# Performance work log

Measured on AMD Instinct MI355X. Metric: run time of the kernel, lower is better.

The kernel has to match this reference:

```python
import jax, jax.numpy as jnp
import numpy as np

EPS_BN = 1e-5
EPS_LN = 1e-5

def _bn(x, g, b, m, v):
    # inference-mode BatchNorm2d over channel dim 1
    scale = g / jnp.sqrt(v + EPS_BN)
    return x * scale[None, :, None, None] + (b - m * scale)[None, :, None, None]

def _conv1x1(x, w, b=None):
    y = jnp.einsum('bchw,oc->bohw', x, w)
    if b is not None:
        y = y + b[None, :, None, None]
    return y

def _gelu(x):
    return jax.nn.gelu(x, approximate=False)

def setup_inputs() -> dict:
    key = jax.random.key(0)
    ks = jax.random.split(key, 40)
    B, C, H, W = 32, 160, 56, 56
    C5, C3 = C // 5, C * 3
    s = 0.05
    d = {}
    d['x'] = jax.random.normal(ks[0], (B, C, H, W), jnp.float32)
    d['bn1_g'] = jax.random.uniform(ks[1], (C,), jnp.float32, 0.5, 1.5)
    d['bn1_b'] = jax.random.normal(ks[2], (C,)) * s
    d['bn1_m'] = jax.random.normal(ks[3], (C,)) * s
    d['bn1_v'] = jnp.ones((C,), jnp.float32)
    names = ['t', 'b', 'r', 'l', 'c']
    for i, n in enumerate(names):
        d['w' + n] = jax.random.normal(ks[4 + i], (C5, C)) * s
        d['b' + n] = jax.random.normal(ks[9 + i], (C5,)) * s
    d['wf1'] = jax.random.normal(ks[14], (C, C)) * s
    d['bf1'] = jax.random.normal(ks[15], (C,)) * s
    d['bn2_g'] = jax.random.uniform(ks[16], (C,), jnp.float32, 0.5, 1.5)
    d['bn2_b'] = jax.random.normal(ks[17], (C,)) * s
    d['bn2_m'] = jax.random.normal(ks[18], (C,)) * s
    d['bn2_v'] = jnp.ones((C,), jnp.float32)
    d['wph'] = jax.random.normal(ks[19], (W, W)) * s
    d['bph'] = jax.random.normal(ks[20], (W,)) * s
    d['wpw'] = jax.random.normal(ks[21], (H, H)) * s
    d['bpw'] = jax.random.normal(ks[22], (H,)) * s
    d['wf2'] = jax.random.normal(ks[23], (C, C3)) * s
    d['ln_g'] = jax.random.uniform(ks[24], (C,), jnp.float32, 0.5, 1.5)
    d['ln_b'] = jax.random.normal(ks[25], (C,)) * s
    d['wfc1'] = jax.random.normal(ks[26], (C3, C)) * s
    d['bfc1'] = jax.random.normal(ks[27], (C3,)) * s
    d['wfc2'] = jax.random.normal(ks[28], (C, C3)) * s
    d['bfc2'] = jax.random.normal(ks[29], (C,)) * s
    d['step'] = 1
    return d

def reference(x, bn1_g, bn1_b, bn1_m, bn1_v, wt, bt, wb, bb, wr, br, wl, bl, wc, bc,
              wf1, bf1, bn2_g, bn2_b, bn2_m, bn2_v, wph, bph, wpw, bpw, wf2,
              ln_g, ln_b, wfc1, bfc1, wfc2, bfc2, step):
    B, C, H, W = x.shape
    # ---- localMix: ShiftedPillarsConcatentation_BNAct_NP5 ----
    h = _gelu(_bn(x, bn1_g, bn1_b, bn1_m, bn1_v))
    x_t = _conv1x1(h, wt, bt)
    x_b = _conv1x1(h, wb, bb)
    x_r = _conv1x1(h, wr, br)
    x_l = _conv1x1(h, wl, bl)
    x_c = _conv1x1(h, wc, bc)
    # pad then narrow exactly as torch: t/l shift by 1, b/r shift by step
    x_t = jnp.pad(x_t, ((0, 0), (0, 0), (0, step), (0, 0)))[:, :, 1:1 + H, :]
    x_b = jnp.pad(x_b, ((0, 0), (0, 0), (step, 0), (0, 0)))[:, :, 0:H, :]
    x_l = jnp.pad(x_l, ((0, 0), (0, 0), (0, 0), (0, step)))[:, :, :, 1:1 + W]
    x_r = jnp.pad(x_r, ((0, 0), (0, 0), (0, 0), (step, 0)))[:, :, :, 0:W]
    lm = _conv1x1(jnp.concatenate([x_t, x_b, x_r, x_l, x_c], axis=1), wf1, bf1)
    # ---- globalMix: sparseMLP_BNAct ----
    g = _gelu(_bn(lm, bn2_g, bn2_b, bn2_m, bn2_v))
    # proj_h mixes the W axis (input permuted to (B,W,C,H)), bias per output W
    x_h = jnp.einsum('bchw,vw->bchv', g, wph) + bph[None, None, None, :]
    # proj_w mixes the H axis (input permuted to (B,H,C,W)), bias per output H
    x_w = jnp.einsum('bchw,uh->bcuw', g, wpw) + bpw[None, None, :, None]
    gm = _conv1x1(jnp.concatenate([g, x_h, x_w], axis=1), wf2)  # no bias
    x1 = gm + x  # residual 1
    # ---- channelMix: LN + Mlp over channels ----
    y = jnp.transpose(x1, (0, 2, 3, 1))  # BHWC
    mu = jnp.mean(y, axis=-1, keepdims=True)
    var = jnp.mean(jnp.square(y - mu), axis=-1, keepdims=True)
    y = (y - mu) / jnp.sqrt(var + EPS_LN) * ln_g + ln_b
    y = _gelu(jnp.einsum('bhwc,fc->bhwf', y, wfc1) + bfc1)
    y = jnp.einsum('bhwf,cf->bhwc', y, wfc2) + bfc2
    return jnp.transpose(y, (0, 3, 1, 2)) + x1  # residual 2
```

## Files before the change

kernel.cpp:

```cpp
#include <hip/hip_runtime.h>
#include <hip/hip_bf16.h>
#include <math.h>

typedef __hip_bfloat16 bf16;
typedef __attribute__((ext_vector_type(8))) short s8v;
typedef __attribute__((ext_vector_type(4))) float f4v;

#define Bn  32
#define Cn  160
#define HWn 3136
#define Pn  100352

__device__ __forceinline__ float b2f(bf16 v){ return __bfloat162float(v); }
__device__ __forceinline__ bf16  f2b(float v){ return __float2bfloat16(v); }
__device__ __forceinline__ float bits2f(unsigned short u){
    union { float f; unsigned int i; } x; x.i = ((unsigned int)u) << 16; return x.f;
}
__device__ __forceinline__ float gelu_f(float x){ return 0.5f*x*(1.0f + erff(x*0.7071067811865476f)); }

#define MFMA(a,b,c) __builtin_amdgcn_mfma_f32_16x16x32_bf16((a),(b),(c),0,0,0)

__global__ __launch_bounds__(256) void k0_prep(
    const float* __restrict__ wt, const float* __restrict__ wb_, const float* __restrict__ wr,
    const float* __restrict__ wl, const float* __restrict__ wc,
    const float* __restrict__ bt, const float* __restrict__ bb_, const float* __restrict__ br,
    const float* __restrict__ bl, const float* __restrict__ bc,
    const float* __restrict__ wf1, const float* __restrict__ bf1,
    const float* __restrict__ g2, const float* __restrict__ b2, const float* __restrict__ m2, const float* __restrict__ v2,
    const float* __restrict__ wf2, const float* __restrict__ wfc1, const float* __restrict__ wfc2,
    const float* __restrict__ wph, const float* __restrict__ wpw,
    const float* __restrict__ lng, const float* __restrict__ lnb, const float* __restrict__ bfc1,
    bf16* wcat, bf16* wf1b, bf16* wf2b, bf16* wfc1g, bf16* wfc2b, bf16* wphb, bf16* wpwb,
    float* bcat, float* epsv, float* eptv, float* wgs, float* wcb)
{
    int idx = blockIdx.x*256 + threadIdx.x;
    if (idx < 25600){ int o = idx/160, k = idx - o*160; int gi = o>>5, oo = o&31;
        const float* wp = gi==0?wt: gi==1?wb_: gi==2?wr: gi==3?wl: wc;
        wcat[idx] = f2b(wp[oo*160+k]); return; }
    idx -= 25600;
    if (idx < 25600){ wf1b[idx] = f2b(wf1[idx]); return; }
    idx -= 25600;
    if (idx < 76800){ wf2b[idx] = f2b(wf2[idx]); return; }
    idx -= 76800;
    if (idx < 76800){ int f = idx/160, c = idx - f*160;
        wfc1g[idx] = f2b(wfc1[f*160+c] * lng[c]); return; }
    idx -= 76800;
    if (idx < 76800){ wfc2b[idx] = f2b(wfc2[idx]); return; }
    idx -= 76800;
    if (idx < 4096){ int v = idx>>6, w = idx&63;
        wphb[idx] = (v<56 && w<56) ? f2b(wph[v*56+w]) : f2b(0.f); return; }
    idx -= 4096;
    if (idx < 4096){ int v = idx>>6, w = idx&63;
        wpwb[idx] = (v<56 && w<56) ? f2b(wpw[v*56+w]) : f2b(0.f); return; }
    idx -= 4096;
    if (idx < 160){ int o = idx; int gi = o>>5, oo = o&31;
        const float* bp = gi==0?bt: gi==1?bb_: gi==2?br: gi==3?bl: bc;
        bcat[o] = bp[oo]; return; }
    idx -= 160;
    if (idx < 160){ int o = idx; float s = g2[o]*rsqrtf(v2[o]+1e-5f);
        epsv[o] = s; eptv[o] = (bf1[o]-m2[o])*s + b2[o]; return; }
    idx -= 160;
    if (idx < 480){ int o = idx; float sg = 0.f, sb = 0.f;
        const float* wr_ = wfc1 + (size_t)o*160;
        for (int c = 0; c < 160; ++c){ float w = wr_[c]; sg += w*lng[c]; sb += w*lnb[c]; }
        wgs[o] = sg; wcb[o] = sb + bfc1[o]; return; }
}

__global__ __launch_bounds__(256) void k1_bn_gelu_tr(const float* __restrict__ x,
    const float* __restrict__ g, const float* __restrict__ b,
    const float* __restrict__ m, const float* __restrict__ v,
    bf16* __restrict__ hT)
{
    __shared__ float tile[64*161];
    __shared__ float sc[160], sh[160];
    int blk = blockIdx.x; int bb = blk/49; int hw0 = (blk - bb*49)*64;
    int tid = threadIdx.x;
    if (tid < 160){
        float s = g[tid] * rsqrtf(v[tid] + 1e-5f);
        sc[tid] = s; sh[tid] = b[tid] - m[tid]*s;
    }
    __syncthreads();
    const float* xb = x + (size_t)bb*Cn*HWn + hw0;
    for (int idx = tid; idx < 160*64; idx += 256){
        int c = idx >> 6, p = idx & 63;
        float val = xb[(size_t)c*HWn + p];
        tile[p*161 + c] = gelu_f(val*sc[c] + sh[c]);
    }
    __syncthreads();
    bf16* ho = hT + ((size_t)bb*HWn + hw0)*Cn;
    for (int idx = tid; idx < 64*160; idx += 256){
        int p = idx/160, c = idx - p*160;
        ho[idx] = f2b(tile[p*161 + c]);
    }
}

__global__ __launch_bounds__(256) void k2_conv5(const bf16* __restrict__ hT,
    const bf16* __restrict__ wcat, const float* __restrict__ bcat, bf16* __restrict__ y5T)
{
    __shared__ __align__(16) unsigned short Bs[2][16*168];
    int tid = threadIdx.x, wave = tid>>6, lane = tid&63, m = lane&15, q = lane>>4;
    size_t pos0 = (size_t)blockIdx.x*64;
    const unsigned short* Ap = (const unsigned short*)hT + (pos0 + wave*16 + m)*160 + q*8;
    s8v a[5];
    #pragma unroll
    for (int kb = 0; kb < 5; ++kb) a[kb] = *(const s8v*)(Ap + kb*32);
    { const s8v* sp = (const s8v*)((const unsigned short*)wcat);
      for (int c = tid; c < 320; c += 256){ int row = c/20, col = (c - row*20)*8;
          *(s8v*)&Bs[0][row*168 + col] = sp[c]; } }
    __syncthreads();
    for (int s = 0; s < 10; ++s){
        if (s+1 < 10){
            const s8v* sp = (const s8v*)((const unsigned short*)wcat + (size_t)(s+1)*2560);
            for (int c = tid; c < 320; c += 256){ int row = c/20, col = (c - row*20)*8;
                *(s8v*)&Bs[(s+1)&1][row*168 + col] = sp[c]; }
        }
        f4v acc = {0.f,0.f,0.f,0.f};
        const unsigned short* Bp = &Bs[s&1][m*168 + q*8];
        #pragma unroll
        for (int kb = 0; kb < 5; ++kb) acc = MFMA(a[kb], *(const s8v*)(Bp + kb*32), acc);
        float bias = bcat[s*16 + m];
        bf16* yo = y5T + (pos0 + wave*16 + q*4)*160 + s*16 + m;
        #pragma unroll
        for (int r = 0; r < 4; ++r) yo[r*160] = f2b(acc[r] + bias);
        __syncthreads();
    }
}

__global__ __launch_bounds__(256) void k3_wf1(const bf16* __restrict__ y5T,
    const bf16* __restrict__ wf1b, const float* __restrict__ epsv, const float* __restrict__ eptv,
    bf16* __restrict__ gT)
{
    __shared__ __align__(16) unsigned short Bs[2][16*168];
    int tid = threadIdx.x, wave = tid>>6, lane = tid&63, m = lane&15, q = lane>>4;
    int blk = blockIdx.x; int bb = blk/49; int hw0 = (blk - bb*49)*64;
    size_t pos0 = (size_t)bb*HWn + hw0;
    int phw = hw0 + wave*16 + m; int h = phw/56, w = phw - h*56;
    s8v a[5];
    #pragma unroll
    for (int kb = 0; kb < 5; ++kb){
        int h2 = h, w2 = w; bool ok = true;
        if      (kb == 0){ h2 = h+1; ok = (h2 < 56); }
        else if (kb == 1){ h2 = h-1; ok = (h2 >= 0); }
        else if (kb == 2){ w2 = w-1; ok = (w2 >= 0); }
        else if (kb == 3){ w2 = w+1; ok = (w2 < 56); }
        if (ok){
            const unsigned short* Ap = (const unsigned short*)y5T +
                ((size_t)bb*HWn + h2*56 + w2)*160 + kb*32 + q*8;
            a[kb] = *(const s8v*)Ap;
        } else {
            a[kb] = (s8v){0,0,0,0,0,0,0,0};
        }
    }
    { const s8v* sp = (const s8v*)((const unsigned short*)wf1b);
      for (int c = tid; c < 320; c += 256){ int row = c/20, col = (c - row*20)*8;
          *(s8v*)&Bs[0][row*168 + col] = sp[c]; } }
    __syncthreads();
    for (int s = 0; s < 10; ++s){
        if (s+1 < 10){
            const s8v* sp = (const s8v*)((const unsigned short*)wf1b + (size_t)(s+1)*2560);
            for (int c = tid; c < 320; c += 256){ int row = c/20, col = (c - row*20)*8;
                *(s8v*)&Bs[(s+1)&1][row*168 + col] = sp[c]; }
        }
        f4v acc = {0.f,0.f,0.f,0.f};
        const unsigned short* Bp = &Bs[s&1][m*168 + q*8];
        #pragma unroll
        for (int kb = 0; kb < 5; ++kb) acc = MFMA(a[kb], *(const s8v*)(Bp + kb*32), acc);
        int o = s*16 + m;
        float es = epsv[o], et = eptv[o];
        bf16* go = gT + (pos0 + wave*16 + q*4)*160 + o;
        #pragma unroll
        for (int r = 0; r < 4; ++r) go[r*160] = f2b(gelu_f(acc[r]*es + et));
        __syncthreads();
    }
}

__global__ __launch_bounds__(256) void k4_projh(const bf16* __restrict__ gT,
    const bf16* __restrict__ wphb, const float* __restrict__ bph, bf16* __restrict__ xhT)
{
    __shared__ __align__(16) unsigned short gS[160*72];
    int tid = threadIdx.x, wave = tid>>6, lane = tid&63, m = lane&15, q = lane>>4;
    int blk = blockIdx.x; int b = blk/56, h = blk - b*56;
    const unsigned short* ga = (const unsigned short*)gT + ((size_t)b*HWn + h*56)*160;
    for (int idx = tid; idx < 56*160; idx += 256){
        int w = idx/160, c = idx - w*160;
        gS[c*72 + w] = ga[idx];
    }
    for (int idx = tid; idx < 160*8; idx += 256){
        int c = idx>>3, w = 56 + (idx&7);
        gS[c*72 + w] = 0;
    }
    __syncthreads();
    int v0 = wave*16;
    s8v a[2];
    #pragma unroll
    for (int kb = 0; kb < 2; ++kb)
        a[kb] = *(const s8v*)((const unsigned short*)wphb + (v0+m)*64 + kb*32 + q*8);
    int v = v0 + q*4;
    for (int s = 0; s < 10; ++s){
        f4v acc = {0.f,0.f,0.f,0.f};
        const unsigned short* Bp = &gS[(s*16+m)*72 + q*8];
        #pragma unroll
        for (int kb = 0; kb < 2; ++kb) acc = MFMA(a[kb], *(const s8v*)(Bp + kb*32), acc);
        #pragma unroll
        for (int r = 0; r < 4; ++r){
            int vv = v + r;
            if (vv < 56)
                xhT[((size_t)b*HWn + h*56 + vv)*160 + s*16 + m] = f2b(acc[r] + bph[vv]);
        }
    }
}

__global__ __launch_bounds__(256) void k5_projw(const bf16* __restrict__ gT,
    const bf16* __restrict__ wpwb, const float* __restrict__ bpw, bf16* __restrict__ xwT)
{
    __shared__ __align__(16) unsigned short gS[160*72];
    int tid = threadIdx.x, wave = tid>>6, lane = tid&63, m = lane&15, q = lane>>4;
    int blk = blockIdx.x; int b = blk/56, w = blk - b*56;
    const unsigned short* gbase = (const unsigned short*)gT + ((size_t)b*HWn + w)*160;
    for (int idx = tid; idx < 56*160; idx += 256){
        int hh = idx/160, c = idx - hh*160;
        gS[c*72 + hh] = gbase[(size_t)hh*56*160 + c];
    }
    for (int idx = tid; idx < 160*8; idx += 256){
        int c = idx>>3, hh = 56 + (idx&7);
        gS[c*72 + hh] = 0;
    }
    __syncthreads();
    int v0 = wave*16;
    s8v a[2];
    #pragma unroll
    for (int kb = 0; kb < 2; ++kb)
        a[kb] = *(const s8v*)((const unsigned short*)wpwb + (v0+m)*64 + kb*32 + q*8);
    int v = v0 + q*4;
    for (int s = 0; s < 10; ++s){
        f4v acc = {0.f,0.f,0.f,0.f};
        const unsigned short* Bp = &gS[(s*16+m)*72 + q*8];
        #pragma unroll
        for (int kb = 0; kb < 2; ++kb) acc = MFMA(a[kb], *(const s8v*)(Bp + kb*32), acc);
        #pragma unroll
        for (int r = 0; r < 4; ++r){
            int vv = v + r;
            if (vv < 56)
                xwT[((size_t)b*HWn + vv*56 + w)*160 + s*16 + m] = f2b(acc[r] + bpw[vv]);
        }
    }
}

__global__ __launch_bounds__(256) void k6_wf2(const bf16* __restrict__ gT,
    const bf16* __restrict__ xhT, const bf16* __restrict__ xwT,
    const bf16* __restrict__ wf2b, bf16* __restrict__ gm)
{
    __shared__ __align__(16) unsigned short Bs[2][16*488];
    int tid = threadIdx.x, wave = tid>>6, lane = tid&63, m = lane&15, q = lane>>4;
    size_t pos0 = (size_t)blockIdx.x*64;
    size_t prow = (pos0 + wave*16 + m)*160;
    s8v a[15];
    #pragma unroll
    for (int kb = 0; kb < 15; ++kb){
        const bf16* src = (kb < 5) ? gT : (kb < 10 ? xhT : xwT);
        int kc = (kb - (kb < 5 ? 0 : (kb < 10 ? 5 : 10)))*32 + q*8;
        a[kb] = *(const s8v*)((const unsigned short*)src + prow + kc);
    }
    { const s8v* sp = (const s8v*)((const unsigned short*)wf2b);
      for (int c = tid; c < 960; c += 256){ int row = c/60, col = (c - row*60)*8;
          *(s8v*)&Bs[0][row*488 + col] = sp[c]; } }
    __syncthreads();
    for (int s = 0; s < 10; ++s){
        if (s+1 < 10){
            const s8v* sp = (const s8v*)((const unsigned short*)wf2b + (size_t)(s+1)*7680);
            for (int c = tid; c < 960; c += 256){ int row = c/60, col = (c - row*60)*8;
                *(s8v*)&Bs[(s+1)&1][row*488 + col] = sp[c]; }
        }
        f4v acc = {0.f,0.f,0.f,0.f};
        const unsigned short* Bp = &Bs[s&1][m*488 + q*8];
        #pragma unroll
        for (int kb = 0; kb < 15; ++kb) acc = MFMA(a[kb], *(const s8v*)(Bp + kb*32), acc);
        bf16* go = gm + (pos0 + wave*16 + q*4)*160 + s*16 + m;
        #pragma unroll
        for (int r = 0; r < 4; ++r) go[r*160] = f2b(acc[r]);
        __syncthreads();
    }
}

__global__ __launch_bounds__(256,4) void k7_ln_fc1(const float* __restrict__ x,
    const bf16* __restrict__ gm,
    const bf16* __restrict__ wfc1g, const float* __restrict__ wgs, const float* __restrict__ wcb,
    bf16* __restrict__ u)
{
    __shared__ __align__(16) float XsU[160*64];
    unsigned short* As = (unsigned short*)XsU;
    float* rstd_s = XsU + 5120;
    float* mrs_s  = XsU + 5184;
    int tid = threadIdx.x, wave = tid>>6, lane = tid&63, m = lane&15, q = lane>>4;
    int blk = blockIdx.x; int bb = blk/49; int hw0 = (blk - bb*49)*64;
    size_t pos0 = (size_t)bb*HWn + hw0;
    const float* xb = x + (size_t)bb*Cn*HWn + hw0;
    for (int idx = tid; idx < 160*64; idx += 256){
        int c = idx >> 6, p = idx & 63;
        XsU[idx] = xb[(size_t)c*HWn + p];
    }
    __syncthreads();
    int p = tid >> 2, q4 = tid & 3;
    {
        const s8v* gp = (const s8v*)((const unsigned short*)gm + (pos0 + p)*160 + q4*40);
        float y[40];
        float s = 0.f, ss = 0.f;
        #pragma unroll
        for (int j = 0; j < 5; ++j){
            s8v gv = gp[j];
            #pragma unroll
            for (int t = 0; t < 8; ++t){
                int i = j*8 + t;
                float vv = XsU[(q4*40 + i)*64 + p] + bits2f((unsigned short)gv[t]);
                y[i] = vv; s += vv; ss += vv*vv;
            }
        }
        s  += __shfl_xor(s, 1);  ss += __shfl_xor(ss, 1);
        s  += __shfl_xor(s, 2);  ss += __shfl_xor(ss, 2);
        float mean = s * (1.f/160.f);
        float var  = ss * (1.f/160.f) - mean*mean;
        float rstd = rsqrtf(var + 1e-5f);
        __syncthreads();
        #pragma unroll
        for (int j = 0; j < 5; ++j){
            s8v pk;
            #pragma unroll
            for (int t = 0; t < 8; ++t){
                union { unsigned short us; bf16 b; } cv; cv.b = f2b(y[j*8 + t]);
                pk[t] = (short)cv.us;
            }
            *(s8v*)&As[p*160 + q4*40 + j*8] = pk;
        }
        if (q4 == 0){ rstd_s[p] = rstd; mrs_s[p] = -mean*rstd; }
    }
    __syncthreads();
    s8v a[5];
    const unsigned short* Ap = &As[(wave*16 + m)*160 + q*8];
    #pragma unroll
    for (int kb = 0; kb < 5; ++kb) a[kb] = *(const s8v*)(Ap + kb*32);
    float rst[4], mrs[4];
    #pragma unroll
    for (int r = 0; r < 4; ++r){
        rst[r] = rstd_s[wave*16 + q*4 + r];
        mrs[r] = mrs_s [wave*16 + q*4 + r];
    }
    const unsigned short* Wp = (const unsigned short*)wfc1g + (size_t)m*160 + q*8;
    bf16* uo = u + (pos0 + wave*16 + q*4)*480 + m;
    s8v b0[5], b1[5];
    #pragma unroll
    for (int kb = 0; kb < 5; ++kb) b0[kb] = *(const s8v*)(Wp + kb*32);
    for (int s = 0; s < 30; s += 2){
        {
            const unsigned short* Wn = Wp + (size_t)(s+1)*2560;
            #pragma unroll
            for (int kb = 0; kb < 5; ++kb) b1[kb] = *(const s8v*)(Wn + kb*32);
        }
        f4v acc = {0.f,0.f,0.f,0.f};
        #pragma unroll
        for (int kb = 0; kb < 5; ++kb) acc = MFMA(a[kb], b0[kb], acc);
        {
            int o = s*16 + m; float wg = wgs[o], wc = wcb[o];
            #pragma unroll
            for (int r = 0; r < 4; ++r){
                float v = acc[r]*rst[r] + mrs[r]*wg + wc;
                uo[(size_t)r*480 + s*16] = f2b(gelu_f(v));
            }
        }
        if (s + 2 < 30){
            const unsigned short* Wn = Wp + (size_t)(s+2)*2560;
            #pragma unroll
            for (int kb = 0; kb < 5; ++kb) b0[kb] = *(const s8v*)(Wn + kb*32);
        }
        f4v acc2 = {0.f,0.f,0.f,0.f};
        #pragma unroll
        for (int kb = 0; kb < 5; ++kb) acc2 = MFMA(a[kb], b1[kb], acc2);
        {
            int o = (s+1)*16 + m; float wg = wgs[o], wc = wcb[o];
            #pragma unroll
            for (int r = 0; r < 4; ++r){
                float v = acc2[r]*rst[r] + mrs[r]*wg + wc;
                uo[(size_t)r*480 + (s+1)*16] = f2b(gelu_f(v));
            }
        }
    }
}

__global__ __launch_bounds__(256) void k8_fc2(const bf16* __restrict__ u,
    const bf16* __restrict__ wfc2b, const float* __restrict__ bfc2,
    const float* __restrict__ x, const bf16* __restrict__ gm, float* __restrict__ out)
{
    __shared__ float Ds[64*161];
    __shared__ __align__(16) unsigned short Bs[2][16*488];
    int tid = threadIdx.x, wave = tid>>6, lane = tid&63, m = lane&15, q = lane>>4;
    int blk = blockIdx.x; int bb = blk/49; int hw0 = (blk - bb*49)*64;
    size_t pos0 = (size_t)bb*HWn + hw0;
    const float* xb = x + (size_t)bb*Cn*HWn + hw0;
    for (int idx = tid; idx < 160*64; idx += 256){
        int o = idx >> 6, p = idx & 63;
        Ds[p*161 + o] = xb[(size_t)o*HWn + p];
    }
    { const s8v* sp = (const s8v*)((const unsigned short*)wfc2b);
      for (int c = tid; c < 960; c += 256){ int row = c/60, col = (c - row*60)*8;
          *(s8v*)&Bs[0][row*488 + col] = sp[c]; } }
    __syncthreads();
    {
        const unsigned short* gp = (const unsigned short*)gm + pos0*160;
        for (int idx = tid; idx < 64*160; idx += 256){
            int p = idx/160, c = idx - p*160;
            Ds[p*161 + c] += bits2f(gp[idx]);
        }
    }
    __syncthreads();
    const unsigned short* Ap = (const unsigned short*)u + (pos0 + wave*16 + m)*480 + q*8;
    s8v a[15];
    #pragma unroll
    for (int kb = 0; kb < 15; ++kb) a[kb] = *(const s8v*)(Ap + kb*32);
    for (int s = 0; s < 10; ++s){
        if (s+1 < 10){
            const s8v* sp = (const s8v*)((const unsigned short*)wfc2b + (size_t)(s+1)*7680);
            for (int c = tid; c < 960; c += 256){ int row = c/60, col = (c - row*60)*8;
                *(s8v*)&Bs[(s+1)&1][row*488 + col] = sp[c]; }
        }
        f4v acc = {0.f,0.f,0.f,0.f};
        const unsigned short* Bp = &Bs[s&1][m*488 + q*8];
        #pragma unroll
        for (int kb = 0; kb < 15; ++kb) acc = MFMA(a[kb], *(const s8v*)(Bp + kb*32), acc);
        int o = s*16 + m; float bias = bfc2[o];
        #pragma unroll
        for (int r = 0; r < 4; ++r)
            Ds[(wave*16 + q*4 + r)*161 + o] += acc[r] + bias;
        __syncthreads();
    }
    float* ob = out + (size_t)bb*Cn*HWn + hw0;
    for (int idx = tid; idx < 160*64; idx += 256){
        int o = idx >> 6, p = idx & 63;
        ob[(size_t)o*HWn + p] = Ds[p*161 + o];
    }
}

extern "C" void kernel_launch(void* const* d_in, const int* in_sizes, int n_in,
                              void* d_out, int out_size, void* d_ws, size_t ws_size,
                              hipStream_t stream)
{
    (void)in_sizes; (void)n_in; (void)out_size; (void)ws_size;
    const float* x     = (const float*)d_in[0];
    const float* bn1g  = (const float*)d_in[1];
    const float* bn1b  = (const float*)d_in[2];
    const float* bn1m  = (const float*)d_in[3];
    const float* bn1v  = (const float*)d_in[4];
    const float* wt    = (const float*)d_in[5];
    const float* bt    = (const float*)d_in[6];
    const float* wb    = (const float*)d_in[7];
    const float* bb    = (const float*)d_in[8];
    const float* wr    = (const float*)d_in[9];
    const float* br    = (const float*)d_in[10];
    const float* wl    = (const float*)d_in[11];
    const float* bl    = (const float*)d_in[12];
    const float* wc    = (const float*)d_in[13];
    const float* bc    = (const float*)d_in[14];
    const float* wf1   = (const float*)d_in[15];
    const float* bf1   = (const float*)d_in[16];
    const float* bn2g  = (const float*)d_in[17];
    const float* bn2b  = (const float*)d_in[18];
    const float* bn2m  = (const float*)d_in[19];
    const float* bn2v  = (const float*)d_in[20];
    const float* wph   = (const float*)d_in[21];
    const float* bph   = (const float*)d_in[22];
    const float* wpw   = (const float*)d_in[23];
    const float* bpw   = (const float*)d_in[24];
    const float* wf2   = (const float*)d_in[25];
    const float* lng   = (const float*)d_in[26];
    const float* lnb   = (const float*)d_in[27];
    const float* wfc1  = (const float*)d_in[28];
    const float* bfc1  = (const float*)d_in[29];
    const float* wfc2  = (const float*)d_in[30];
    const float* bfc2v = (const float*)d_in[31];
    float* outp = (float*)d_out;

    const size_t PC2 = (size_t)Pn*160*2;
    char* ws = (char*)d_ws;
    bf16* hT   = (bf16*)(ws + 0*PC2);
    bf16* y5T  = (bf16*)(ws + 1*PC2);
    bf16* gT   = (bf16*)(ws + 2*PC2);
    bf16* xhT  = (bf16*)(ws + 3*PC2);
    bf16* xwT  = (bf16*)(ws + 4*PC2);
    bf16* gm   = (bf16*)(ws + 5*PC2);
    char* wsw  = ws + 6*PC2;
    bf16*  wcat  = (bf16*)(wsw + 0);
    bf16*  wf1b  = (bf16*)(wsw + 51200);
    bf16*  wf2b  = (bf16*)(wsw + 102400);
    bf16*  wfc1g = (bf16*)(wsw + 256000);
    bf16*  wfc2b = (bf16*)(wsw + 409600);
    bf16*  wphb  = (bf16*)(wsw + 563200);
    bf16*  wpwb  = (bf16*)(wsw + 571392);
    float* bcat  = (float*)(wsw + 579584);
    float* epsv  = (float*)(wsw + 580224);
    float* eptv  = (float*)(wsw + 580864);
    float* wgs   = (float*)(wsw + 581504);
    float* wcb   = (float*)(wsw + 583424);
    bf16* uB   = (bf16*)(ws + 0);

    const int GP = Pn/64;
    const int GS = Bn*56;

    k0_prep<<<1136, 256, 0, stream>>>(wt, wb, wr, wl, wc, bt, bb, br, bl, bc,
                                      wf1, bf1, bn2g, bn2b, bn2m, bn2v,
                                      wf2, wfc1, wfc2, wph, wpw,
                                      lng, lnb, bfc1,
                                      wcat, wf1b, wf2b, wfc1g, wfc2b, wphb, wpwb,
                                      bcat, epsv, eptv, wgs, wcb);
    k1_bn_gelu_tr<<<GP, 256, 0, stream>>>(x, bn1g, bn1b, bn1m, bn1v, hT);
    k2_conv5     <<<GP, 256, 0, stream>>>(hT, wcat, bcat, y5T);
    k3_wf1       <<<GP, 256, 0, stream>>>(y5T, wf1b, epsv, eptv, gT);
    k4_projh     <<<GS, 256, 0, stream>>>(gT, wphb, bph, xhT);
    k5_projw     <<<GS, 256, 0, stream>>>(gT, wpwb, bpw, xwT);
    k6_wf2       <<<GP, 256, 0, stream>>>(gT, xhT, xwT, wf2b, gm);
    k7_ln_fc1    <<<GP, 256, 0, stream>>>(x, gm, wfc1g, wgs, wcb, uB);
    k8_fc2       <<<GP, 256, 0, stream>>>(uB, wfc2b, bfc2v, x, gm, outp);
}
```

Before: 506.6 us.

## Fuse LayerNorm+fc1 and fc2 kernels into one MLP kernel keeping hidden in LDS

```diff
diff --git a/kernel.cpp b/kernel.cpp
--- a/kernel.cpp
+++ b/kernel.cpp
@@ -5,6 +5,7 @@
 typedef __hip_bfloat16 bf16;
 typedef __attribute__((ext_vector_type(8))) short s8v;
 typedef __attribute__((ext_vector_type(4))) float f4v;
+typedef __attribute__((ext_vector_type(4))) unsigned short u4v;
 
 #define Bn  32
 #define Cn  160
@@ -15,6 +16,9 @@
 __device__ __forceinline__ bf16  f2b(float v){ return __float2bfloat16(v); }
 __device__ __forceinline__ float bits2f(unsigned short u){
     union { float f; unsigned int i; } x; x.i = ((unsigned int)u) << 16; return x.f;
+}
+__device__ __forceinline__ unsigned short f2bits(float v){
+    union { unsigned short us; bf16 b; } cv; cv.b = f2b(v); return cv.us;
 }
 __device__ __forceinline__ float gelu_f(float x){ return 0.5f*x*(1.0f + erff(x*0.7071067811865476f)); }
 
@@ -282,159 +286,128 @@
     }
 }
 
-__global__ __launch_bounds__(256,4) void k7_ln_fc1(const float* __restrict__ x,
+__global__ __launch_bounds__(256,3) void k78_mlp(const float* __restrict__ x,
     const bf16* __restrict__ gm,
     const bf16* __restrict__ wfc1g, const float* __restrict__ wgs, const float* __restrict__ wcb,
-    bf16* __restrict__ u)
-{
-    __shared__ __align__(16) float XsU[160*64];
-    unsigned short* As = (unsigned short*)XsU;
-    float* rstd_s = XsU + 5120;
-    float* mrs_s  = XsU + 5184;
-    int tid = threadIdx.x, wave = tid>>6, lane = tid&63, m = lane&15, q = lane>>4;
-    int blk = blockIdx.x; int bb = blk/49; int hw0 = (blk - bb*49)*64;
+    const bf16* __restrict__ wfc2b, const float* __restrict__ bfc2,
+    float* __restrict__ out)
+{
+    __shared__ __align__(16) char lds[41728];
+    float* Xs = (float*)lds;
+    unsigned short* Us = (unsigned short*)lds;
+    unsigned short* As = (unsigned short*)(lds + 31232);
+    float* rstd_s = (float*)(lds + 41472);
+    float* mrs_s  = (float*)(lds + 41600);
+
+    int tid = threadIdx.x, wave = tid>>6, lane = tid&63, m = lane&15, q = lane>>4;
+    int rt = wave&1, chh = wave>>1;
+    int blk = blockIdx.x; int bb = blk/98; int hw0 = (blk - bb*98)*32;
     size_t pos0 = (size_t)bb*HWn + hw0;
     const float* xb = x + (size_t)bb*Cn*HWn + hw0;
-    for (int idx = tid; idx < 160*64; idx += 256){
-        int c = idx >> 6, p = idx & 63;
-        XsU[idx] = xb[(size_t)c*HWn + p];
-    }
-    __syncthreads();
-    int p = tid >> 2, q4 = tid & 3;
+
+    for (int idx = tid; idx < 160*32; idx += 256){
+        int c = idx >> 5, p = idx & 31;
+        Xs[p*164 + c] = xb[(size_t)c*HWn + p];
+    }
+    __syncthreads();
+
     {
-        const s8v* gp = (const s8v*)((const unsigned short*)gm + (pos0 + p)*160 + q4*40);
-        float y[40];
-        float s = 0.f, ss = 0.f;
+        int p = tid >> 3, q8 = tid & 7; int c0 = q8*20;
+        const unsigned short* gp = (const unsigned short*)gm + (pos0 + p)*160 + c0;
+        float y[20]; float s = 0.f, ss = 0.f;
         #pragma unroll
         for (int j = 0; j < 5; ++j){
-            s8v gv = gp[j];
-            #pragma unroll
-            for (int t = 0; t < 8; ++t){
-                int i = j*8 + t;
-                float vv = XsU[(q4*40 + i)*64 + p] + bits2f((unsigned short)gv[t]);
-                y[i] = vv; s += vv; ss += vv*vv;
+            u4v gv = *(const u4v*)(gp + j*4);
+            f4v xv = *(const f4v*)&Xs[p*164 + c0 + j*4];
+            #pragma unroll
+            for (int t = 0; t < 4; ++t){
+                float vv = xv[t] + bits2f(gv[t]);
+                y[j*4 + t] = vv; s += vv; ss += vv*vv;
             }
         }
-        s  += __shfl_xor(s, 1);  ss += __shfl_xor(ss, 1);
-        s  += __shfl_xor(s, 2);  ss += __shfl_xor(ss, 2);
+        s += __shfl_xor(s, 1); ss += __shfl_xor(ss, 1);
+        s += __shfl_xor(s, 2); ss += __shfl_xor(ss, 2);
+        s += __shfl_xor(s, 4); ss += __shfl_xor(ss, 4);
         float mean = s * (1.f/160.f);
         float var  = ss * (1.f/160.f) - mean*mean;
         float rstd = rsqrtf(var + 1e-5f);
-        __syncthreads();
         #pragma unroll
         for (int j = 0; j < 5; ++j){
-            s8v pk;
-            #pragma unroll
-            for (int t = 0; t < 8; ++t){
-                union { unsigned short us; bf16 b; } cv; cv.b = f2b(y[j*8 + t]);
-                pk[t] = (short)cv.us;
+            u4v pk;
+            #pragma unroll
+            for (int t = 0; t < 4; ++t) pk[t] = f2bits(y[j*4 + t]);
+            *(u4v*)&As[p*160 + c0 + j*4] = pk;
+        }
+        if (q8 == 0){ rstd_s[p] = rstd; mrs_s[p] = -mean*rstd; }
+    }
+    __syncthreads();
+
+    {
+        s8v a1[5];
+        #pragma unroll
+        for (int kb = 0; kb < 5; ++kb)
+            a1[kb] = *(const s8v*)&As[(rt*16 + m)*160 + q*8 + kb*32];
+        float rst[4], mrs[4];
+        #pragma unroll
+        for (int r = 0; r < 4; ++r){
+            rst[r] = rstd_s[rt*16 + q*4 + r];
+            mrs[r] = mrs_s [rt*16 + q*4 + r];
+        }
+        const unsigned short* W1 = (const unsigned short*)wfc1g + ((size_t)chh*15*16 + m)*160 + q*8;
+        s8v b0[5], b1[5];
+        #pragma unroll
+        for (int kb = 0; kb < 5; ++kb) b0[kb] = *(const s8v*)(W1 + kb*32);
+        #pragma unroll
+        for (int s = 0; s < 15; ++s){
+            if (s + 1 < 15){
+                const unsigned short* Wn = W1 + (size_t)(s+1)*2560;
+                #pragma unroll
+                for (int kb = 0; kb < 5; ++kb) b1[kb] = *(const s8v*)(Wn + kb*32);
             }
-            *(s8v*)&As[p*160 + q4*40 + j*8] = pk;
-        }
-        if (q4 == 0){ rstd_s[p] = rstd; mrs_s[p] = -mean*rstd; }
-    }
-    __syncthreads();
-    s8v a[5];
-    const unsigned short* Ap = &As[(wave*16 + m)*160 + q*8];
-    #pragma unroll
-    for (int kb = 0; kb < 5; ++kb) a[kb] = *(const s8v*)(Ap + kb*32);
-    float rst[4], mrs[4];
-    #pragma unroll
-    for (int r = 0; r < 4; ++r){
-        rst[r] = rstd_s[wave*16 + q*4 + r];
-        mrs[r] = mrs_s [wave*16 + q*4 + r];
-    }
-    const unsigned short* Wp = (const unsigned short*)wfc1g + (size_t)m*160 + q*8;
-    bf16* uo = u + (pos0 + wave*16 + q*4)*480 + m;
-    s8v b0[5], b1[5];
-    #pragma unroll
-    for (int kb = 0; kb < 5; ++kb) b0[kb] = *(const s8v*)(Wp + kb*32);
-    for (int s = 0; s < 30; s += 2){
-        {
-            const unsigned short* Wn = Wp + (size_t)(s+1)*2560;
-            #pragma unroll
-            for (int kb = 0; kb < 5; ++kb) b1[kb] = *(const s8v*)(Wn + kb*32);
-        }
-        f4v acc = {0.f,0.f,0.f,0.f};
-        #pragma unroll
-        for (int kb = 0; kb < 5; ++kb) acc = MFMA(a[kb], b0[kb], acc);
-        {
-            int o = s*16 + m; float wg = wgs[o], wc = wcb[o];
+            f4v acc = {0.f,0.f,0.f,0.f};
+            #pragma unroll
+            for (int kb = 0; kb < 5; ++kb) acc = MFMA(a1[kb], b0[kb], acc);
+            int o = (chh*15 + s)*16 + m;
+            float wg = wgs[o], wc = wcb[o];
             #pragma unroll
             for (int r = 0; r < 4; ++r){
                 float v = acc[r]*rst[r] + mrs[r]*wg + wc;
-                uo[(size_t)r*480 + s*16] = f2b(gelu_f(v));
+                Us[(rt*16 + q*4 + r)*488 + o] = f2bits(gelu_f(v));
             }
-        }
-        if (s + 2 < 30){
-            const unsigned short* Wn = Wp + (size_t)(s+2)*2560;
-            #pragma unroll
-            for (int kb = 0; kb < 5; ++kb) b0[kb] = *(const s8v*)(Wn + kb*32);
-        }
-        f4v acc2 = {0.f,0.f,0.f,0.f};
-        #pragma unroll
-        for (int kb = 0; kb < 5; ++kb) acc2 = MFMA(a[kb], b1[kb], acc2);
-        {
-            int o = (s+1)*16 + m; float wg = wgs[o], wc = wcb[o];
-            #pragma unroll
-            for (int r = 0; r < 4; ++r){
-                float v = acc2[r]*rst[r] + mrs[r]*wg + wc;
-                uo[(size_t)r*480 + (s+1)*16] = f2b(gelu_f(v));
+            if (s + 1 < 15){
+                #pragma unroll
+                for (int kb = 0; kb < 5; ++kb) b0[kb] = b1[kb];
             }
         }
     }
-}
-
-__global__ __launch_bounds__(256) void k8_fc2(const bf16* __restrict__ u,
-    const bf16* __restrict__ wfc2b, const float* __restrict__ bfc2,
-    const float* __restrict__ x, const bf16* __restrict__ gm, float* __restrict__ out)
-{
-    __shared__ float Ds[64*161];
-    __shared__ __align__(16) unsigned short Bs[2][16*488];
-    int tid = threadIdx.x, wave = tid>>6, lane = tid&63, m = lane&15, q = lane>>4;
-    int blk = blockIdx.x; int bb = blk/49; int hw0 = (blk - bb*49)*64;
-    size_t pos0 = (size_t)bb*HWn + hw0;
-    const float* xb = x + (size_t)bb*Cn*HWn + hw0;
-    for (int idx = tid; idx < 160*64; idx += 256){
-        int o = idx >> 6, p = idx & 63;
-        Ds[p*161 + o] = xb[(size_t)o*HWn + p];
-    }
-    { const s8v* sp = (const s8v*)((const unsigned short*)wfc2b);
-      for (int c = tid; c < 960; c += 256){ int row = c/60, col = (c - row*60)*8;
-          *(s8v*)&Bs[0][row*488 + col] = sp[c]; } }
-    __syncthreads();
+    __syncthreads();
+
     {
-        const unsigned short* gp = (const unsigned short*)gm + pos0*160;
-        for (int idx = tid; idx < 64*160; idx += 256){
-            int p = idx/160, c = idx - p*160;
-            Ds[p*161 + c] += bits2f(gp[idx]);
-        }
-    }
-    __syncthreads();
-    const unsigned short* Ap = (const unsigned short*)u + (pos0 + wave*16 + m)*480 + q*8;
-    s8v a[15];
-    #pragma unroll
-    for (int kb = 0; kb < 15; ++kb) a[kb] = *(const s8v*)(Ap + kb*32);
-    for (int s = 0; s < 10; ++s){
-        if (s+1 < 10){
-            const s8v* sp = (const s8v*)((const unsigned short*)wfc2b + (size_t)(s+1)*7680);
-            for (int c = tid; c < 960; c += 256){ int row = c/60, col = (c - row*60)*8;
-                *(s8v*)&Bs[(s+1)&1][row*488 + col] = sp[c]; }
-        }
-        f4v acc = {0.f,0.f,0.f,0.f};
-        const unsigned short* Bp = &Bs[s&1][m*488 + q*8];
-        #pragma unroll
-        for (int kb = 0; kb < 15; ++kb) acc = MFMA(a[kb], *(const s8v*)(Bp + kb*32), acc);
-        int o = s*16 + m; float bias = bfc2[o];
-        #pragma unroll
-        for (int r = 0; r < 4; ++r)
-            Ds[(wave*16 + q*4 + r)*161 + o] += acc[r] + bias;
-        __syncthreads();
-    }
-    float* ob = out + (size_t)bb*Cn*HWn + hw0;
-    for (int idx = tid; idx < 160*64; idx += 256){
-        int o = idx >> 6, p = idx & 63;
-        ob[(size_t)o*HWn + p] = Ds[p*161 + o];
+        s8v a2[15];
+        #pragma unroll
+        for (int kb = 0; kb < 15; ++kb)
+            a2[kb] = *(const s8v*)&Us[(rt*16 + m)*488 + q*8 + kb*32];
+        #pragma unroll
+        for (int s = 0; s < 5; ++s){
+            int o = chh*80 + s*16 + m;
+            const unsigned short* W2 = (const unsigned short*)wfc2b + (size_t)o*480 + q*8;
+            s8v b2[15];
+            #pragma unroll
+            for (int kb = 0; kb < 15; ++kb) b2[kb] = *(const s8v*)(W2 + kb*32);
+            f4v acc = {0.f,0.f,0.f,0.f};
+            #pragma unroll
+            for (int kb = 0; kb < 15; ++kb) acc = MFMA(a2[kb], b2[kb], acc);
+            float bias = bfc2[o];
+            const float* xp = x + (size_t)bb*Cn*HWn + (size_t)o*HWn + hw0 + rt*16 + q*4;
+            f4v x4 = *(const f4v*)xp;
+            const unsigned short* gmp = (const unsigned short*)gm + (pos0 + rt*16 + q*4)*160 + o;
+            f4v o4;
+            #pragma unroll
+            for (int r = 0; r < 4; ++r)
+                o4[r] = x4[r] + bits2f(gmp[(size_t)r*160]) + acc[r] + bias;
+            float* op = out + (size_t)bb*Cn*HWn + (size_t)o*HWn + hw0 + rt*16 + q*4;
+            *(f4v*)op = o4;
+        }
     }
 }
 
@@ -498,10 +471,10 @@
     float* eptv  = (float*)(wsw + 580864);
     float* wgs   = (float*)(wsw + 581504);
     float* wcb   = (float*)(wsw + 583424);
-    bf16* uB   = (bf16*)(ws + 0);
 
     const int GP = Pn/64;
     const int GS = Bn*56;
+    const int GF = Pn/32;
 
     k0_prep<<<1136, 256, 0, stream>>>(wt, wb, wr, wl, wc, bt, bb, br, bl, bc,
                                       wf1, bf1, bn2g, bn2b, bn2m, bn2v,
@@ -515,6 +488,5 @@
     k4_projh     <<<GS, 256, 0, stream>>>(gT, wphb, bph, xhT);
     k5_projw     <<<GS, 256, 0, stream>>>(gT, wpwb, bpw, xwT);
     k6_wf2       <<<GP, 256, 0, stream>>>(gT, xhT, xwT, wf2b, gm);
-    k7_ln_fc1    <<<GP, 256, 0, stream>>>(x, gm, wfc1g, wgs, wcb, uB);
-    k8_fc2       <<<GP, 256, 0, stream>>>(uB, wfc2b, bfc2v, x, gm, outp);
-}
+    k78_mlp      <<<GF, 256, 0, stream>>>(x, gm, wfc1g, wgs, wcb, wfc2b, bfc2v, outp);
+}
```

Result: faster. 478.1 us (-5.6%).
